# Performance work log

Measured on AMD Instinct MI355X. Metric: run time of the kernel, lower is better.

The kernel has to match this reference:

```python
import jax, jax.numpy as jnp
import numpy as np

B, T, D, H = 64, 512, 256, 512

def _xavier(key, shape):
    fan_in, fan_out = shape
    lim = np.sqrt(6.0 / (fan_in + fan_out))
    return jax.random.uniform(key, shape, jnp.float32, -lim, lim)

def setup_inputs() -> dict:
    key = jax.random.key(0)
    ks = jax.random.split(key, 16)
    inp = {
        'x': jax.random.normal(ks[0], (B, T, D), jnp.float32),
        'h': jax.random.normal(ks[1], (B, H), jnp.float32),
        'We2h': _xavier(ks[2], (D, H)),            # err_in2h (no bias)
        'Wr_x': _xavier(ks[3], (D, H)),
        'Wr_h': _xavier(ks[4], (H, H)),
        'Wr_e': _xavier(ks[5], (H, H)),
        'br': jnp.zeros((H,), jnp.float32),
        'Wz_x': _xavier(ks[6], (D, H)),
        'Wz_h': _xavier(ks[7], (H, H)),
        'Wz_e': _xavier(ks[8], (H, H)),
        'bz': jnp.ones((H,), jnp.float32),         # update_bias.fill_(1.0)
        'Wn_x': _xavier(ks[9], (D, H)),
        'Wn_h': _xavier(ks[10], (H, H)),
        'Wn_e': _xavier(ks[11], (H, H)),
        'bn': jnp.zeros((H,), jnp.float32),
        'Wo': _xavier(ks[12], (H, D)),             # readout Linear(H, D)
        'bo': jnp.zeros((D,), jnp.float32),
    }
    return inp

def reference(x, h, We2h, Wr_x, Wr_h, Wr_e, br, Wz_x, Wz_h, Wz_e, bz, Wn_x, Wn_h, Wn_e, bn, Wo, bo):
    # Precompute all input-to-hidden projections in large GEMMs: [B,T,H]
    x_e = jnp.einsum('btd,dh->bth', x, We2h)
    x_r = jnp.einsum('btd,dh->bth', x, Wr_x) + br
    x_z = jnp.einsum('btd,dh->bth', x, Wz_x) + bz
    x_n = jnp.einsum('btd,dh->bth', x, Wn_x) + bn
    # scan over time: inputs [T,B,H]
    xs = (jnp.swapaxes(x_e, 0, 1), jnp.swapaxes(x_r, 0, 1),
          jnp.swapaxes(x_z, 0, 1), jnp.swapaxes(x_n, 0, 1))

    def step(h, ins):
        xe_t, xr_t, xz_t, xn_t = ins
        e = xe_t - h                                   # innovation e_t
        r = jax.nn.sigmoid(xr_t + h @ Wr_h + e @ Wr_e)
        z = jax.nn.sigmoid(xz_t + h @ Wz_h + e @ Wz_e)
        n = jnp.tanh(xn_t + (r * h) @ Wn_h + (r * e) @ Wn_e)
        h_new = (1.0 - z) * h + z * n
        return h_new, h_new

    _, h_seq = jax.lax.scan(step, h, xs)               # [T,B,H]
    h_seq = jnp.swapaxes(h_seq, 0, 1)                  # [B,T,H]
    out = jnp.einsum('bth,hd->btd', h_seq, Wo) + bo    # [B,T,D]
    return out, h_seq
```

## Files before the change

kernel.cpp:

```cpp
#include <hip/hip_runtime.h>
#include <hip/hip_bf16.h>
#include <hip/hip_fp16.h>

#define B_ 64
#define T_ 512
#define D_ 256
#define H_ 512
#define M_ (B_*T_)

#define NBLK 64
#define JO 8

typedef unsigned int uint;
typedef __attribute__((ext_vector_type(8))) short bf16x8;
typedef __attribute__((ext_vector_type(4))) float f32x4;
typedef _Float16 half_t;
typedef __attribute__((ext_vector_type(2))) _Float16 half2_t;

__device__ __forceinline__ unsigned short f32_to_bf16(float f) {
    unsigned u = __builtin_bit_cast(unsigned, f);
    unsigned r = (u + 0x7fffu + ((u >> 16) & 1u)) >> 16;
    return (unsigned short)r;
}
__device__ __forceinline__ float bf16_to_f32(unsigned short h) {
    unsigned u = ((unsigned)h) << 16;
    return __builtin_bit_cast(float, u);
}
__device__ __forceinline__ unsigned pkh2(float a, float b) {
    half2_t h; h.x = (half_t)a; h.y = (half_t)b;
    return __builtin_bit_cast(unsigned, h);
}
__device__ __forceinline__ half2_t uph2(unsigned u) {
    return __builtin_bit_cast(half2_t, u);
}

#if __has_builtin(__builtin_amdgcn_fdot2)
__device__ __forceinline__ float fdot2(half2_t a, half2_t b, float c) {
    return __builtin_amdgcn_fdot2(a, b, c, false);
}
#else
__device__ __forceinline__ float fdot2(half2_t a, half2_t b, float c) {
    return c + (float)a.x * (float)b.x + (float)a.y * (float)b.y;
}
#endif

__device__ __forceinline__ uint ald(const uint* p) {
    return __hip_atomic_load(p, __ATOMIC_RELAXED, __HIP_MEMORY_SCOPE_AGENT);
}
__device__ __forceinline__ void ast(uint* p, uint v) {
    __hip_atomic_store(p, v, __ATOMIC_RELAXED, __HIP_MEMORY_SCOPE_AGENT);
}

__device__ __forceinline__ float sigmoidf_(float x) {
    return 1.f / (1.f + __expf(-x));
}

__device__ __forceinline__ void gbar(uint* cnt, uint target, int tid) {
    __syncthreads();
    if (tid == 0) {
        asm volatile("s_waitcnt vmcnt(0)" ::: "memory");
        __hip_atomic_fetch_add(cnt, 1u, __ATOMIC_RELAXED, __HIP_MEMORY_SCOPE_AGENT);
        int it = 0;
        while (__hip_atomic_load(cnt, __ATOMIC_RELAXED, __HIP_MEMORY_SCOPE_AGENT) < target) {
            if (++it > (1 << 22)) break;
            __builtin_amdgcn_s_sleep(1);
        }
    }
    __syncthreads();
}

__global__ void comp_p(const float* __restrict__ We2h, const float* __restrict__ Wre,
                       const float* __restrict__ Wze,
                       float* __restrict__ Pr, float* __restrict__ Pz) {
    int tid = blockIdx.x * blockDim.x + threadIdx.x;
    if (tid >= 256 * 512) return;
    int k = tid >> 9, j = tid & 511;
    float ar = 0.f, az = 0.f;
    for (int kk = 0; kk < 512; kk++) {
        float e = We2h[k * 512 + kk];
        ar += e * Wre[kk * 512 + j];
        az += e * Wze[kk * 512 + j];
    }
    Pr[tid] = ar;
    Pz[tid] = az;
}

__global__ void build_wt(const float* __restrict__ We2h, const float* __restrict__ Wrx,
                         const float* __restrict__ Wzx, const float* __restrict__ Wnx,
                         const float* __restrict__ Pr, const float* __restrict__ Pz,
                         const float* __restrict__ br, const float* __restrict__ bz,
                         const float* __restrict__ bn, const float* __restrict__ Wo,
                         unsigned short* __restrict__ WcatT, float* __restrict__ biascat,
                         unsigned short* __restrict__ WoT) {
    int tid = blockIdx.x * blockDim.x + threadIdx.x;
    const int total1 = 2048 * 256;
    if (tid < total1) {
        int n = tid >> 8, k = tid & 255;
        int sel = n >> 9, nl = n & 511;
        float v;
        if (sel == 0)      v = We2h[k * 512 + nl];
        else if (sel == 1) v = Wrx[k * 512 + nl] + Pr[k * 512 + nl];
        else if (sel == 2) v = Wzx[k * 512 + nl] + Pz[k * 512 + nl];
        else               v = Wnx[k * 512 + nl];
        WcatT[tid] = f32_to_bf16(v);
        if (k == 0) {
            float bv = sel == 0 ? 0.f : sel == 1 ? br[nl] : sel == 2 ? bz[nl] : bn[nl];
            biascat[n] = bv;
        }
    } else {
        int t2 = tid - total1;
        if (t2 < 256 * 512) {
            int n = t2 >> 9, k = t2 & 511;
            WoT[t2] = f32_to_bf16(Wo[k * 256 + n]);
        }
    }
}

__global__ void build_wscan(const float* __restrict__ Wrh, const float* __restrict__ Wre,
                            const float* __restrict__ Wzh, const float* __restrict__ Wze,
                            const float* __restrict__ Wnh, const float* __restrict__ Wne,
                            uint2* __restrict__ warz, uint* __restrict__ wan) {
    int tid = blockIdx.x * blockDim.x + threadIdx.x;
    if (tid < 256 * 512) {
        int kp = tid >> 9, j = tid & 511;
        int k0 = 2 * kp;
        float ar0 = Wrh[k0 * 512 + j] - Wre[k0 * 512 + j];
        float ar1 = Wrh[(k0 + 1) * 512 + j] - Wre[(k0 + 1) * 512 + j];
        float az0 = Wzh[k0 * 512 + j] - Wze[k0 * 512 + j];
        float az1 = Wzh[(k0 + 1) * 512 + j] - Wze[(k0 + 1) * 512 + j];
        warz[tid] = make_uint2(pkh2(ar0, ar1), pkh2(az0, az1));
    }
    int t2 = tid - 256 * 512;
    if (t2 >= 0 && t2 < 512 * 512) {
        int k = t2 >> 9, j = t2 & 511;
        float an = Wnh[k * 512 + j] - Wne[k * 512 + j];
        wan[t2] = pkh2(an, Wne[k * 512 + j]);
    }
}

__global__ void init_hbuf(const float* __restrict__ h0, uint* __restrict__ hbuf) {
    int tid = blockIdx.x * blockDim.x + threadIdx.x;
    if (tid >= 256 * 64) return;
    int kp = tid >> 6, m = tid & 63;
    hbuf[tid] = pkh2(h0[m * 512 + 2 * kp], h0[m * 512 + 2 * kp + 1]);
}

__global__ __launch_bounds__(256)
void gemmx_kernel(const float* __restrict__ A, const unsigned short* __restrict__ BT,
                  const float* __restrict__ bias, unsigned short* __restrict__ xT) {
    __shared__ unsigned short Asm[128 * 64];
    __shared__ unsigned short Bsm[128 * 64];
    __shared__ unsigned short Csm[128][128];
    const int tid = threadIdx.x;
    const int t0 = blockIdx.x * 2;
    const int c0 = blockIdx.y * 128;
    const int lane = tid & 63, wid = tid >> 6;
    const int wm = wid >> 1, wn = wid & 1;
    const int lr = lane & 15, lg = lane >> 4;

    f32x4 acc[4][4] = {};

    const int srow = tid >> 1, shalf = tid & 1;
    const int rowA = (srow & 63) * 512 + t0 + (srow >> 6);
    const float* Arow = A + (size_t)rowA * 256 + shalf * 32;
    const unsigned short* Brow = BT + (size_t)(c0 + srow) * 256 + shalf * 32;
    unsigned short* As = &Asm[srow * 64 + shalf * 32];
    unsigned short* Bs = &Bsm[srow * 64 + shalf * 32];

    for (int kt = 0; kt < 256; kt += 64) {
#pragma unroll
        for (int q = 0; q < 8; q++) {
            float4 v = *(const float4*)(Arow + kt + q * 4);
            unsigned p0 = ((unsigned)f32_to_bf16(v.y) << 16) | f32_to_bf16(v.x);
            unsigned p1 = ((unsigned)f32_to_bf16(v.w) << 16) | f32_to_bf16(v.z);
            *(uint2*)(As + q * 4) = make_uint2(p0, p1);
        }
#pragma unroll
        for (int q = 0; q < 4; q++) {
            uint4 v = *(const uint4*)(Brow + kt + q * 8);
            *(uint4*)(Bs + q * 8) = v;
        }
        __syncthreads();
#pragma unroll
        for (int ks = 0; ks < 2; ks++) {
            bf16x8 af[4], bfr[4];
#pragma unroll
            for (int m = 0; m < 4; m++)
                af[m] = *(const bf16x8*)&Asm[(wm * 64 + m * 16 + lr) * 64 + ks * 32 + lg * 8];
#pragma unroll
            for (int n2 = 0; n2 < 4; n2++)
                bfr[n2] = *(const bf16x8*)&Bsm[(wn * 64 + n2 * 16 + lr) * 64 + ks * 32 + lg * 8];
#pragma unroll
            for (int m = 0; m < 4; m++)
#pragma unroll
                for (int n2 = 0; n2 < 4; n2++)
                    acc[m][n2] = __builtin_amdgcn_mfma_f32_16x16x32_bf16(
                        af[m], bfr[n2], acc[m][n2], 0, 0, 0);
        }
        __syncthreads();
    }
#pragma unroll
    for (int m = 0; m < 4; m++) {
        int r0 = wm * 64 + m * 16 + lg * 4;
#pragma unroll
        for (int n2 = 0; n2 < 4; n2++) {
            int c = wn * 64 + n2 * 16 + lr;
            float bv = bias[c0 + c];
#pragma unroll
            for (int i = 0; i < 4; i++)
                Csm[c][r0 + i] = f32_to_bf16(acc[m][n2][i] + bv);
        }
    }
    __syncthreads();
#pragma unroll
    for (int th = 0; th < 2; th++) {
        uint4* dst = (uint4*)(xT + ((size_t)(t0 + th) * 2048 + c0) * 64);
        for (int q = tid; q < 1024; q += 256) {
            int c = q >> 3, b0 = (q & 7) * 8;
            dst[q] = *(const uint4*)&Csm[c][th * 64 + b0];
        }
        __syncthreads();
    }
}

__global__ __launch_bounds__(256)
void gemm_out_kernel(const float* __restrict__ A, const unsigned short* __restrict__ BT,
                     const float* __restrict__ bias, float* __restrict__ C,
                     int M, int N, int K) {
    __shared__ unsigned short Asm[128 * 64];
    __shared__ unsigned short Bsm[128 * 64];
    const int tid = threadIdx.x;
    const int bm = blockIdx.x, bn = blockIdx.y;
    const int lane = tid & 63, wid = tid >> 6;
    const int wm = wid >> 1, wn = wid & 1;
    const int lr = lane & 15, lg = lane >> 4;

    f32x4 acc[4][4] = {};

    const int srow = tid >> 1, shalf = tid & 1;
    const float* Arow = A + (size_t)(bm * 128 + srow) * K + shalf * 32;
    const unsigned short* Brow = BT + (size_t)(bn * 128 + srow) * K + shalf * 32;
    unsigned short* As = &Asm[srow * 64 + shalf * 32];
    unsigned short* Bs = &Bsm[srow * 64 + shalf * 32];

    for (int kt = 0; kt < K; kt += 64) {
#pragma unroll
        for (int q = 0; q < 8; q++) {
            float4 v = *(const float4*)(Arow + kt + q * 4);
            unsigned p0 = ((unsigned)f32_to_bf16(v.y) << 16) | f32_to_bf16(v.x);
            unsigned p1 = ((unsigned)f32_to_bf16(v.w) << 16) | f32_to_bf16(v.z);
            *(uint2*)(As + q * 4) = make_uint2(p0, p1);
        }
#pragma unroll
        for (int q = 0; q < 4; q++) {
            uint4 v = *(const uint4*)(Brow + kt + q * 8);
            *(uint4*)(Bs + q * 8) = v;
        }
        __syncthreads();
#pragma unroll
        for (int ks = 0; ks < 2; ks++) {
            bf16x8 af[4], bfr[4];
#pragma unroll
            for (int m = 0; m < 4; m++)
                af[m] = *(const bf16x8*)&Asm[(wm * 64 + m * 16 + lr) * 64 + ks * 32 + lg * 8];
#pragma unroll
            for (int n2 = 0; n2 < 4; n2++)
                bfr[n2] = *(const bf16x8*)&Bsm[(wn * 64 + n2 * 16 + lr) * 64 + ks * 32 + lg * 8];
#pragma unroll
            for (int m = 0; m < 4; m++)
#pragma unroll
                for (int n2 = 0; n2 < 4; n2++)
                    acc[m][n2] = __builtin_amdgcn_mfma_f32_16x16x32_bf16(
                        af[m], bfr[n2], acc[m][n2], 0, 0, 0);
        }
        __syncthreads();
    }
#pragma unroll
    for (int m = 0; m < 4; m++) {
        int row0 = bm * 128 + wm * 64 + m * 16 + lg * 4;
#pragma unroll
        for (int n2 = 0; n2 < 4; n2++) {
            int col = bn * 128 + wn * 64 + n2 * 16 + lr;
            float bv = bias[col];
#pragma unroll
            for (int i = 0; i < 4; i++)
                C[(size_t)(row0 + i) * N + col] = acc[m][n2][i] + bv;
        }
    }
}

__global__ __launch_bounds__(512)
void scan_sync(const unsigned short* __restrict__ xT,
               const float* __restrict__ h0,
               const uint2* __restrict__ warz,
               const uint* __restrict__ wan,
               uint* __restrict__ hbuf,
               uint* __restrict__ rhrxe,
               uint* __restrict__ cnts,
               float* __restrict__ hseq)
{
    __shared__ uint2 Wrz_l[256][JO];
    __shared__ uint  Wn_l[512][JO];
    __shared__ float part[3][8][JO][64];
    __shared__ float h_loc[JO][64], z_loc[JO][64];

    const int bid = blockIdx.x, tid = threadIdx.x;
    const int lane = tid & 63, wv = tid >> 6;
    const int j0 = bid * JO;
    const int jF = tid >> 6, mF = tid & 63;

    uint* cnt0 = cnts;
    uint* cnt1 = cnts + 32;

    for (int i = tid; i < 256 * JO; i += 512) {
        int kp = i >> 3, j = i & 7;
        Wrz_l[kp][j] = warz[kp * 512 + j0 + j];
    }
    for (int i = tid; i < 512 * JO; i += 512) {
        int k = i >> 3, j = i & 7;
        Wn_l[k][j] = wan[k * 512 + j0 + j];
    }
    h_loc[jF][mF] = h0[mF * 512 + j0 + jF];
    __syncthreads();

    for (int t = 0; t < T_; t++) {
        const int jg = j0 + jF;
        const size_t xbase = (size_t)t * 2048 * 64;
        float xe = bf16_to_f32(xT[xbase + (size_t)jg * 64 + mF]);
        float xr = bf16_to_f32(xT[xbase + (size_t)(512 + jg) * 64 + mF]);
        float xz = bf16_to_f32(xT[xbase + (size_t)(1024 + jg) * 64 + mF]);
        float xn = bf16_to_f32(xT[xbase + (size_t)(1536 + jg) * 64 + mF]);

        {
            uint hv[32];
#pragma unroll
            for (int q = 0; q < 32; q++)
                hv[q] = ald(&hbuf[(wv * 32 + q) * 64 + lane]);
            float ar[JO] = {}, az[JO] = {};
#pragma unroll
            for (int q = 0; q < 32; q++) {
                half2_t h2 = uph2(hv[q]);
#pragma unroll
                for (int j = 0; j < JO; j++) {
                    uint2 w = *(const uint2*)&Wrz_l[wv * 32 + q][j];
                    ar[j] = fdot2(h2, uph2(w.x), ar[j]);
                    az[j] = fdot2(h2, uph2(w.y), az[j]);
                }
            }
#pragma unroll
            for (int j = 0; j < JO; j++) {
                part[0][wv][j][lane] = ar[j];
                part[1][wv][j][lane] = az[j];
            }
        }
        __syncthreads();

        {
            float sr = 0.f, sz = 0.f;
#pragma unroll
            for (int w = 0; w < 8; w++) { sr += part[0][w][jF][mF]; sz += part[1][w][jF][mF]; }
            float r = sigmoidf_(xr + sr);
            float z = sigmoidf_(xz + sz);
            float h = h_loc[jF][mF];
            z_loc[jF][mF] = z;
            ast(&rhrxe[jg * 64 + mF], pkh2(r * h, r * xe));
        }
        gbar(cnt0, (uint)(t + 1) * NBLK, tid);

        {
            float an[JO] = {};
#pragma unroll
            for (int ch = 0; ch < 2; ch++) {
                uint rv[32];
#pragma unroll
                for (int q = 0; q < 32; q++)
                    rv[q] = ald(&rhrxe[(wv * 64 + ch * 32 + q) * 64 + lane]);
#pragma unroll
                for (int q = 0; q < 32; q++) {
                    half2_t p2 = uph2(rv[q]);
#pragma unroll
                    for (int j = 0; j < JO; j++)
                        an[j] = fdot2(p2, uph2(Wn_l[wv * 64 + ch * 32 + q][j]), an[j]);
                }
            }
#pragma unroll
            for (int j = 0; j < JO; j++) part[2][wv][j][lane] = an[j];
        }
        __syncthreads();

        {
            float sn = 0.f;
#pragma unroll
            for (int w = 0; w < 8; w++) sn += part[2][w][jF][mF];
            float nn = tanhf(xn + sn);
            float z = z_loc[jF][mF];
            float h = h_loc[jF][mF];
            h_loc[jF][mF] = (1.f - z) * h + z * nn;
        }
        __syncthreads();

        if (tid < (JO / 2) * 64) {
            int jp = tid >> 6, mh = tid & 63;
            ast(&hbuf[(bid * (JO / 2) + jp) * 64 + mh],
                pkh2(h_loc[2 * jp][mh], h_loc[2 * jp + 1][mh]));
        }
        {
            int js = tid & 7, ms = tid >> 3;
            hseq[((size_t)ms * 512 + t) * 512 + j0 + js] = h_loc[js][ms];
        }
        gbar(cnt1, (uint)(t + 1) * NBLK, tid);
    }
}

extern "C" void kernel_launch(void* const* d_in, const int* in_sizes, int n_in,
                              void* d_out, int out_size, void* d_ws, size_t ws_size,
                              hipStream_t stream) {
    const float* x    = (const float*)d_in[0];
    const float* h0   = (const float*)d_in[1];
    const float* We2h = (const float*)d_in[2];
    const float* Wrx  = (const float*)d_in[3];
    const float* Wrh  = (const float*)d_in[4];
    const float* Wre  = (const float*)d_in[5];
    const float* br   = (const float*)d_in[6];
    const float* Wzx  = (const float*)d_in[7];
    const float* Wzh  = (const float*)d_in[8];
    const float* Wze  = (const float*)d_in[9];
    const float* bz   = (const float*)d_in[10];
    const float* Wnx  = (const float*)d_in[11];
    const float* Wnh  = (const float*)d_in[12];
    const float* Wne  = (const float*)d_in[13];
    const float* bn   = (const float*)d_in[14];
    const float* Wo   = (const float*)d_in[15];
    const float* bo   = (const float*)d_in[16];

    char* w = (char*)d_ws;
    unsigned short* xT    = (unsigned short*)(w);
    uint2*          warz  = (uint2*)(w + 134217728);
    uint*           wan   = (uint*)(w + 135266304);
    unsigned short* WcatT = (unsigned short*)(w + 136314880);
    unsigned short* WoT   = (unsigned short*)(w + 137363456);
    float*          biascat = (float*)(w + 137625600);
    float*          Pr    = (float*)(w + 137633792);
    float*          Pz    = (float*)(w + 138158080);
    uint*           hbuf  = (uint*)(w + 138682368);
    uint*           rhrxe = (uint*)(w + 138747904);
    uint*           cnts  = (uint*)(w + 138878976);

    float* out  = (float*)d_out;
    float* hseq = (float*)d_out + (size_t)M_ * D_;

    hipMemsetAsync(cnts, 0, 256, stream);

    comp_p<<<(256 * 512 + 255) / 256, 256, 0, stream>>>(We2h, Wre, Wze, Pr, Pz);
    build_wt<<<(2048 * 256 + 256 * 512 + 255) / 256, 256, 0, stream>>>(
        We2h, Wrx, Wzx, Wnx, Pr, Pz, br, bz, bn, Wo, WcatT, biascat, WoT);
    build_wscan<<<(256 * 512 + 512 * 512 + 255) / 256, 256, 0, stream>>>(
        Wrh, Wre, Wzh, Wze, Wnh, Wne, warz, wan);
    init_hbuf<<<(256 * 64 + 255) / 256, 256, 0, stream>>>(h0, hbuf);

    {
        dim3 grid(T_ / 2, 2048 / 128);
        gemmx_kernel<<<grid, 256, 0, stream>>>(x, WcatT, biascat, xT);
    }
    scan_sync<<<NBLK, 512, 0, stream>>>(xT, h0, warz, wan, hbuf, rhrxe, cnts, hseq);
    {
        dim3 grid(M_ / 128, D_ / 128);
        gemm_out_kernel<<<grid, 256, 0, stream>>>(hseq, WoT, bo, out, M_, D_, H_);
    }
}
```

Measured before the change: 5.893 ms.

## Use hierarchical grid barrier with per-group flags and prefetch next-step inputs

Replaces the single shared grid-barrier counter with a two-level barrier. Blocks first count on one of 8 group counters spaced on separate cache lines; the last arriver of each group bumps a root counter, and the final arriver releases per-group flags that each group polls. This is meant to cut atomic and polling contention on one address across 64 blocks, at the cost of an extra serial atomic hop and a longer sleep interval. It also loads the next timestep's precomputed input projections before the second barrier, so that load latency is hidden behind the wait.

```diff
diff --git a/kernel.cpp b/kernel.cpp
--- a/kernel.cpp
+++ b/kernel.cpp
@@ -10,6 +10,7 @@
 
 #define NBLK 64
 #define JO 8
+#define BAR_STRIDE 2048
 
 typedef unsigned int uint;
 typedef __attribute__((ext_vector_type(8))) short bf16x8;
@@ -55,15 +56,28 @@
     return 1.f / (1.f + __expf(-x));
 }
 
-__device__ __forceinline__ void gbar(uint* cnt, uint target, int tid) {
+__device__ __forceinline__ void gbar2(uint* base, uint t, int tid, int bid) {
     __syncthreads();
     if (tid == 0) {
         asm volatile("s_waitcnt vmcnt(0)" ::: "memory");
-        __hip_atomic_fetch_add(cnt, 1u, __ATOMIC_RELAXED, __HIP_MEMORY_SCOPE_AGENT);
+        const uint g = (uint)bid & 7u;
+        uint old = __hip_atomic_fetch_add(&base[g * 64], 1u,
+                      __ATOMIC_RELAXED, __HIP_MEMORY_SCOPE_AGENT);
+        if (old == t * 8u + 7u) {
+            uint r = __hip_atomic_fetch_add(&base[512], 1u,
+                      __ATOMIC_RELAXED, __HIP_MEMORY_SCOPE_AGENT);
+            if (r == t * 8u + 7u) {
+#pragma unroll
+                for (int e = 0; e < 8; e++)
+                    __hip_atomic_store(&base[640 + e * 64], t + 1u,
+                      __ATOMIC_RELAXED, __HIP_MEMORY_SCOPE_AGENT);
+            }
+        }
         int it = 0;
-        while (__hip_atomic_load(cnt, __ATOMIC_RELAXED, __HIP_MEMORY_SCOPE_AGENT) < target) {
+        while (__hip_atomic_load(&base[640 + g * 64],
+                 __ATOMIC_RELAXED, __HIP_MEMORY_SCOPE_AGENT) < t + 1u) {
             if (++it > (1 << 22)) break;
-            __builtin_amdgcn_s_sleep(1);
+            __builtin_amdgcn_s_sleep(2);
         }
     }
     __syncthreads();
@@ -309,8 +323,8 @@
     const int j0 = bid * JO;
     const int jF = tid >> 6, mF = tid & 63;
 
-    uint* cnt0 = cnts;
-    uint* cnt1 = cnts + 32;
+    uint* bar0 = cnts;
+    uint* bar1 = cnts + BAR_STRIDE;
 
     for (int i = tid; i < 256 * JO; i += 512) {
         int kp = i >> 3, j = i & 7;
@@ -323,14 +337,14 @@
     h_loc[jF][mF] = h0[mF * 512 + j0 + jF];
     __syncthreads();
 
+    const int jg = j0 + jF;
+    const size_t xoff = (size_t)jg * 64 + mF;
+    float xe = bf16_to_f32(xT[xoff]);
+    float xr = bf16_to_f32(xT[xoff + (size_t)512 * 64]);
+    float xz = bf16_to_f32(xT[xoff + (size_t)1024 * 64]);
+    float xn = bf16_to_f32(xT[xoff + (size_t)1536 * 64]);
+
     for (int t = 0; t < T_; t++) {
-        const int jg = j0 + jF;
-        const size_t xbase = (size_t)t * 2048 * 64;
-        float xe = bf16_to_f32(xT[xbase + (size_t)jg * 64 + mF]);
-        float xr = bf16_to_f32(xT[xbase + (size_t)(512 + jg) * 64 + mF]);
-        float xz = bf16_to_f32(xT[xbase + (size_t)(1024 + jg) * 64 + mF]);
-        float xn = bf16_to_f32(xT[xbase + (size_t)(1536 + jg) * 64 + mF]);
-
         {
             uint hv[32];
 #pragma unroll
@@ -365,7 +379,7 @@
             z_loc[jF][mF] = z;
             ast(&rhrxe[jg * 64 + mF], pkh2(r * h, r * xe));
         }
-        gbar(cnt0, (uint)(t + 1) * NBLK, tid);
+        gbar2(bar0, (uint)t, tid, bid);
 
         {
             float an[JO] = {};
@@ -408,7 +422,17 @@
             int js = tid & 7, ms = tid >> 3;
             hseq[((size_t)ms * 512 + t) * 512 + j0 + js] = h_loc[js][ms];
         }
-        gbar(cnt1, (uint)(t + 1) * NBLK, tid);
+
+        float xe2 = 0.f, xr2 = 0.f, xz2 = 0.f, xn2 = 0.f;
+        if (t + 1 < T_) {
+            const size_t xb = (size_t)(t + 1) * 2048 * 64 + xoff;
+            xe2 = bf16_to_f32(xT[xb]);
+            xr2 = bf16_to_f32(xT[xb + (size_t)512 * 64]);
+            xz2 = bf16_to_f32(xT[xb + (size_t)1024 * 64]);
+            xn2 = bf16_to_f32(xT[xb + (size_t)1536 * 64]);
+        }
+        gbar2(bar1, (uint)t, tid, bid);
+        xe = xe2; xr = xr2; xz = xz2; xn = xn2;
     }
 }
 
@@ -449,7 +473,7 @@
     float* out  = (float*)d_out;
     float* hseq = (float*)d_out + (size_t)M_ * D_;
 
-    hipMemsetAsync(cnts, 0, 256, stream);
+    hipMemsetAsync(cnts, 0, 2 * BAR_STRIDE * sizeof(uint), stream);
 
     comp_p<<<(256 * 512 + 255) / 256, 256, 0, stream>>>(We2h, Wre, Wze, Pr, Pz);
     build_wt<<<(2048 * 256 + 256 * 512 + 255) / 256, 256, 0, stream>>>(
```

New measurement: 5.690 ms. 3.5% less time.

## Replace atomic-counter grid barrier with per-block flag array and prefetch scan inputs

Applied to the files above, without the earlier changes.

The grid barrier in the recurrent scan no longer has every block atomically increment one shared counter. Each block now stores the phase number into its own padded flag slot, and one wavefront polls all 64 flags in parallel with a wave-wide vote. This removes contention on a single counter and the sleep-based polling. The per-step projected inputs for the next timestep are also loaded before the barrier, so their global-load latency overlaps the wait. The cost is dropping the explicit vmcnt wait before the flag store, which may weaken the ordering of the hbuf/rhrxe writes relative to the flag.

```diff
diff --git a/kernel.cpp b/kernel.cpp
--- a/kernel.cpp
+++ b/kernel.cpp
@@ -55,18 +55,21 @@
     return 1.f / (1.f + __expf(-x));
 }
 
-__device__ __forceinline__ void gbar(uint* cnt, uint target, int tid) {
+__device__ __forceinline__ void gbar(uint* flags, uint target, int tid, int bid) {
     __syncthreads();
-    if (tid == 0) {
-        asm volatile("s_waitcnt vmcnt(0)" ::: "memory");
-        __hip_atomic_fetch_add(cnt, 1u, __ATOMIC_RELAXED, __HIP_MEMORY_SCOPE_AGENT);
+    if (tid < 64) {
+        if (tid == 0)
+            __hip_atomic_store(&flags[bid * 4], target,
+                               __ATOMIC_RELAXED, __HIP_MEMORY_SCOPE_AGENT);
         int it = 0;
-        while (__hip_atomic_load(cnt, __ATOMIC_RELAXED, __HIP_MEMORY_SCOPE_AGENT) < target) {
-            if (++it > (1 << 22)) break;
-            __builtin_amdgcn_s_sleep(1);
-        }
-    }
-    __syncthreads();
+        uint f;
+        do {
+            f = __hip_atomic_load(&flags[tid * 4],
+                                  __ATOMIC_RELAXED, __HIP_MEMORY_SCOPE_AGENT);
+            if (++it > (1 << 24)) break;
+        } while (!__all(f >= target));
+    }
+    __builtin_amdgcn_s_barrier();
 }
 
 __global__ void comp_p(const float* __restrict__ We2h, const float* __restrict__ Wre,
@@ -296,7 +299,7 @@
                const uint* __restrict__ wan,
                uint* __restrict__ hbuf,
                uint* __restrict__ rhrxe,
-               uint* __restrict__ cnts,
+               uint* __restrict__ flags,
                float* __restrict__ hseq)
 {
     __shared__ uint2 Wrz_l[256][JO];
@@ -309,9 +312,6 @@
     const int j0 = bid * JO;
     const int jF = tid >> 6, mF = tid & 63;
 
-    uint* cnt0 = cnts;
-    uint* cnt1 = cnts + 32;
-
     for (int i = tid; i < 256 * JO; i += 512) {
         int kp = i >> 3, j = i & 7;
         Wrz_l[kp][j] = warz[kp * 512 + j0 + j];
@@ -323,14 +323,14 @@
     h_loc[jF][mF] = h0[mF * 512 + j0 + jF];
     __syncthreads();
 
+    const int jg = j0 + jF;
+    const size_t xoff = (size_t)jg * 64 + mF;
+    unsigned short pxe = xT[xoff];
+    unsigned short pxr = xT[xoff + (size_t)512 * 64];
+    unsigned short pxz = xT[xoff + (size_t)1024 * 64];
+    unsigned short pxn = xT[xoff + (size_t)1536 * 64];
+
     for (int t = 0; t < T_; t++) {
-        const int jg = j0 + jF;
-        const size_t xbase = (size_t)t * 2048 * 64;
-        float xe = bf16_to_f32(xT[xbase + (size_t)jg * 64 + mF]);
-        float xr = bf16_to_f32(xT[xbase + (size_t)(512 + jg) * 64 + mF]);
-        float xz = bf16_to_f32(xT[xbase + (size_t)(1024 + jg) * 64 + mF]);
-        float xn = bf16_to_f32(xT[xbase + (size_t)(1536 + jg) * 64 + mF]);
-
         {
             uint hv[32];
 #pragma unroll
@@ -355,17 +355,18 @@
         }
         __syncthreads();
 
+        float xe = bf16_to_f32(pxe), xn_f = bf16_to_f32(pxn);
         {
             float sr = 0.f, sz = 0.f;
 #pragma unroll
             for (int w = 0; w < 8; w++) { sr += part[0][w][jF][mF]; sz += part[1][w][jF][mF]; }
-            float r = sigmoidf_(xr + sr);
-            float z = sigmoidf_(xz + sz);
+            float r = sigmoidf_(bf16_to_f32(pxr) + sr);
+            float z = sigmoidf_(bf16_to_f32(pxz) + sz);
             float h = h_loc[jF][mF];
             z_loc[jF][mF] = z;
             ast(&rhrxe[jg * 64 + mF], pkh2(r * h, r * xe));
         }
-        gbar(cnt0, (uint)(t + 1) * NBLK, tid);
+        gbar(flags, 2u * (uint)t + 1u, tid, bid);
 
         {
             float an[JO] = {};
@@ -392,7 +393,7 @@
             float sn = 0.f;
 #pragma unroll
             for (int w = 0; w < 8; w++) sn += part[2][w][jF][mF];
-            float nn = tanhf(xn + sn);
+            float nn = tanhf(xn_f + sn);
             float z = z_loc[jF][mF];
             float h = h_loc[jF][mF];
             h_loc[jF][mF] = (1.f - z) * h + z * nn;
@@ -408,7 +409,29 @@
             int js = tid & 7, ms = tid >> 3;
             hseq[((size_t)ms * 512 + t) * 512 + j0 + js] = h_loc[js][ms];
         }
-        gbar(cnt1, (uint)(t + 1) * NBLK, tid);
+
+        __syncthreads();
+        if (t + 1 < T_) {
+            const size_t xb = (size_t)(t + 1) * 2048 * 64 + xoff;
+            pxe = xT[xb];
+            pxr = xT[xb + (size_t)512 * 64];
+            pxz = xT[xb + (size_t)1024 * 64];
+            pxn = xT[xb + (size_t)1536 * 64];
+        }
+        __builtin_amdgcn_sched_barrier(0);
+        if (tid < 64) {
+            if (tid == 0)
+                __hip_atomic_store(&flags[bid * 4], 2u * (uint)t + 2u,
+                                   __ATOMIC_RELAXED, __HIP_MEMORY_SCOPE_AGENT);
+            int it = 0;
+            uint f;
+            do {
+                f = __hip_atomic_load(&flags[tid * 4],
+                                      __ATOMIC_RELAXED, __HIP_MEMORY_SCOPE_AGENT);
+                if (++it > (1 << 24)) break;
+            } while (!__all(f >= 2u * (uint)t + 2u));
+        }
+        __builtin_amdgcn_s_barrier();
     }
 }
 
@@ -444,12 +467,12 @@
     float*          Pz    = (float*)(w + 138158080);
     uint*           hbuf  = (uint*)(w + 138682368);
     uint*           rhrxe = (uint*)(w + 138747904);
-    uint*           cnts  = (uint*)(w + 138878976);
+    uint*           flags = (uint*)(w + 138878976);
 
     float* out  = (float*)d_out;
     float* hseq = (float*)d_out + (size_t)M_ * D_;
 
-    hipMemsetAsync(cnts, 0, 256, stream);
+    hipMemsetAsync(flags, 0, NBLK * 4 * sizeof(uint), stream);
 
     comp_p<<<(256 * 512 + 255) / 256, 256, 0, stream>>>(We2h, Wre, Wze, Pr, Pz);
     build_wt<<<(2048 * 256 + 256 * 512 + 255) / 256, 256, 0, stream>>>(
@@ -462,7 +485,7 @@
         dim3 grid(T_ / 2, 2048 / 128);
         gemmx_kernel<<<grid, 256, 0, stream>>>(x, WcatT, biascat, xT);
     }
-    scan_sync<<<NBLK, 512, 0, stream>>>(xT, h0, warz, wan, hbuf, rhrxe, cnts, hseq);
+    scan_sync<<<NBLK, 512, 0, stream>>>(xT, h0, warz, wan, hbuf, rhrxe, flags, hseq);
     {
         dim3 grid(M_ / 128, D_ / 128);
         gemm_out_kernel<<<grid, 256, 0, stream>>>(hseq, WoT, bo, out, M_, D_, H_);
```

After: 5.560 ms. 1.06x faster.
